# Kernel optimization log

Measured on AMD Instinct MI355X. Metric: run time of the kernel, lower is better.

Reference implementation:

```python
import jax, jax.numpy as jnp
import numpy as np

N, D = 768, 64
EPS = 1e-5

def _ln(x, g, b):
    u = x.mean(-1, keepdims=True)
    s = ((x - u) ** 2).mean(-1, keepdims=True)
    return g * (x - u) / jnp.sqrt(s + EPS) + b

def setup_inputs() -> dict:
    key = jax.random.key(0)
    ks = jax.random.split(key, 16)
    inp = {
        'corr_index': jax.random.normal(ks[0], (N, N, 2), dtype=jnp.float32),
        'nei_index': jax.random.randint(ks[1], (N, N), 0, 2, dtype=jnp.int32),
        'nei_num': jax.random.randint(ks[2], (N,), 0, N, dtype=jnp.int32),
        'hidden_state': jax.random.normal(ks[3], (N, D), dtype=jnp.float32),
        'cn': jax.random.normal(ks[4], (N, D), dtype=jnp.float32),
        # relativeLayer: MLP(2 -> D)
        'W_r': jax.random.normal(ks[5], (2, D)) * 0.01, 'b_r': jnp.zeros((D,)),
        'g_r': jnp.ones((D,)), 'be_r': jax.random.normal(ks[6], (D,)) * 0.02,
        # ngate: MLP_gate(3D -> D)
        'W_g': jax.random.normal(ks[7], (3 * D, D)) * 0.01, 'b_g': jnp.zeros((D,)),
        'g_g': jnp.ones((D,)), 'be_g': jax.random.normal(ks[8], (D,)) * 0.02,
        # WAr: MLP(3D -> 1)
        'W_a': jax.random.normal(ks[9], (3 * D, 1)) * 0.01, 'b_a': jnp.zeros((1,)),
        'g_a': jnp.ones((1,)), 'be_a': jnp.abs(jax.random.normal(ks[10], (1,))) * 0.02 + 0.01,
        # weight: MLP(D -> D)
        'W_w': jax.random.normal(ks[11], (D, D)) * 0.01, 'b_w': jnp.zeros((D,)),
        'g_w': jnp.ones((D,)), 'be_w': jax.random.normal(ks[12], (D,)) * 0.02,
    }
    return inp

def reference(corr_index, nei_index, nei_num, hidden_state, cn,
              W_r, b_r, g_r, be_r, W_g, b_g, g_g, be_g,
              W_a, b_a, g_a, be_a, W_w, b_w, g_w, be_w):
    n, d = hidden_state.shape
    mask = nei_index > 0  # [N,N]; (i,j): j is neighbor of i
    # relativeLayer on all pairs (values at masked positions match the torch gather)
    r = jax.nn.relu(_ln(corr_index @ W_r + b_r, g_r, be_r))  # [N,N,D]
    hi = jnp.broadcast_to(hidden_state[:, None, :], (n, n, d))  # hi_t: h[i]
    hj = jnp.broadcast_to(hidden_state[None, :, :], (n, n, d))  # nei_inputs: h[j]
    tmp = jnp.concatenate([r, hi, hj], axis=-1)  # [N,N,3D]
    nGate = jax.nn.sigmoid(_ln(tmp @ W_g + b_g, g_g, be_g))  # [N,N,D]
    tt = jax.nn.relu(_ln(tmp @ W_a + b_a, g_a, be_a))[..., 0]  # [N,N]
    Pos = jnp.where(mask, tt, 0.0)
    Pos = jnp.where(Pos == 0.0, -10000.0, Pos)  # Pos[Pos==0] = -10000
    Pos = jax.nn.softmax(Pos, axis=1)  # masked row-softmax over neighbors j
    # H[i,j] = h[j] * nGate[i,j] * Pos[i,j] at masked pairs, else 0
    H = jnp.where(mask[..., None], hj * nGate * Pos[..., None], 0.0)
    H_sum = jax.nn.relu(_ln(jnp.sum(H, axis=1) @ W_w + b_w, g_w, be_w))  # [N,D]
    C = H_sum + cn
    H_out = hidden_state + jnp.tanh(C)
    return (H_out, C)
```

## Files before the change

### kernel.cpp

```cpp
#include <hip/hip_runtime.h>


#define NN 768
#define DD 64
#define NCH 12
#define EPSF 1e-5f

typedef __attribute__((ext_vector_type(8))) short short8;
typedef __attribute__((ext_vector_type(4))) float float4v;

__device__ __forceinline__ unsigned short f2bf(float f) {
  unsigned int u = __float_as_uint(f);
  u += 0x7fffu + ((u >> 16) & 1u);
  return (unsigned short)(u >> 16);
}

__global__ __launch_bounds__(256) void prep_kernel(
    const float* __restrict__ hidden, const float* __restrict__ Wg,
    const float* __restrict__ bg, const float* __restrict__ Wr,
    const float* __restrict__ br, const int* __restrict__ nei,
    float* __restrict__ A_pre, float* __restrict__ B_pre,
    float* __restrict__ w0h, float* __restrict__ w1h, float* __restrict__ bh,
    float* __restrict__ evec, unsigned short* __restrict__ WgT,
    unsigned short* __restrict__ Lst, int* __restrict__ cnt_g) {
  const int bid = blockIdx.x;
  const int tid = threadIdx.x;

  if (bid < NN) {
    __shared__ int cLds;
    if (tid == 0) cLds = 0;
    __syncthreads();
#pragma unroll
    for (int rep = 0; rep < 3; ++rep) {
      int jj = tid + rep * 256;
      if (nei[bid * NN + jj] > 0) {
        int idx = atomicAdd(&cLds, 1);
        Lst[bid * NN + idx] = (unsigned short)jj;
      }
    }
    __syncthreads();
    if (tid == 0) cnt_g[bid] = cLds;
    return;
  }

  if (bid == NN) {
    for (int idx = tid; idx < DD * DD; idx += 256) {
      int n = idx >> 6, k = idx & 63;
      WgT[idx] = f2bf(Wg[k * DD + n]);
    }
    if (tid < 64) {
      int t = tid;
      float w0 = Wr[t], w1 = Wr[DD + t], bb = br[t];
      float m0 = w0, m1 = w1, mb = bb;
      for (int m = 1; m < 64; m <<= 1) {
        m0 += __shfl_xor(m0, m);
        m1 += __shfl_xor(m1, m);
        mb += __shfl_xor(mb, m);
      }
      m0 *= (1.f / DD);
      m1 *= (1.f / DD);
      mb *= (1.f / DD);
      float a0 = w0 - m0, a1 = w1 - m1, ab = bb - mb;
      w0h[t] = a0;
      w1h[t] = a1;
      bh[t] = ab;
      float e00 = a0 * a0, e11 = a1 * a1, ebb = ab * ab;
      float e01 = a0 * a1, e0b = a0 * ab, e1b = a1 * ab;
      for (int m = 1; m < 64; m <<= 1) {
        e00 += __shfl_xor(e00, m);
        e11 += __shfl_xor(e11, m);
        ebb += __shfl_xor(ebb, m);
        e01 += __shfl_xor(e01, m);
        e0b += __shfl_xor(e0b, m);
        e1b += __shfl_xor(e1b, m);
      }
      if (t == 0) {
        evec[0] = e00 * (1.f / DD);
        evec[1] = e11 * (1.f / DD);
        evec[2] = ebb * (1.f / DD);
        evec[3] = e01 * (1.f / DD);
        evec[4] = e0b * (1.f / DD);
        evec[5] = e1b * (1.f / DD);
      }
    }
    return;
  }

  const int w = tid >> 6;
  const int lane = tid & 63;
  const int i = (bid - NN - 1) * 4 + w;
  float hv = hidden[i * DD + lane];
  float a = bg[lane];
  float b = 0.f;
#pragma unroll 8
  for (int k = 0; k < DD; ++k) {
    float hk = __shfl(hv, k);
    a = fmaf(hk, Wg[(DD + k) * DD + lane], a);
    b = fmaf(hk, Wg[(2 * DD + k) * DD + lane], b);
  }
  A_pre[i * DD + lane] = a;
  B_pre[i * DD + lane] = b;
}

__global__ __launch_bounds__(64) void pair_kernel(
    const float* __restrict__ corr, const float* __restrict__ hidden,
    const float* __restrict__ gr, const float* __restrict__ ber,
    const float* __restrict__ gg, const float* __restrict__ beg,
    const float* __restrict__ A_pre, const float* __restrict__ B_pre,
    const float* __restrict__ w0h, const float* __restrict__ w1h,
    const float* __restrict__ bh, const float* __restrict__ evec,
    const unsigned short* __restrict__ WgT,
    const unsigned short* __restrict__ Lst, const int* __restrict__ cnt_g,
    float* __restrict__ Hpart) {
  const int bid = blockIdx.x;
  const int i = bid / NCH;
  const int c = bid - i * NCH;
  const int cnt = cnt_g[i];
  const int base = c * 64;
  if (base >= cnt) return;

  const int lane = threadIdx.x;
  const int quad = lane >> 4;
  const int nl = lane & 15;

  __shared__ __align__(16) unsigned short Rt[64 * 72];
  __shared__ int jpc[64];

  int pg = base + lane;
  int jp = (int)Lst[i * NN + (pg < cnt ? pg : base)];
  jpc[lane] = jp;
  float c0 = corr[(i * NN + jp) * 2 + 0];
  float c1 = corr[(i * NN + jp) * 2 + 1];
  const float e00 = evec[0], e11 = evec[1], ebb = evec[2];
  const float e01 = evec[3], e0b = evec[4], e1b = evec[5];
  float var = c0 * c0 * e00 + c1 * c1 * e11 + ebb +
              2.f * (c0 * c1 * e01 + c0 * e0b + c1 * e1b);
  float iv = rsqrtf(var + EPSF);

  const float pgr = gr[lane];
  const float gw0 = pgr * w0h[lane];
  const float gw1 = pgr * w1h[lane];
  const float gbh = pgr * bh[lane];
  const float pber = ber[lane];

  short8 Bf[2][4];
#pragma unroll
  for (int ks = 0; ks < 2; ++ks)
#pragma unroll
    for (int nt = 0; nt < 4; ++nt)
      __builtin_memcpy(&Bf[ks][nt], &WgT[(nt * 16 + nl) * DD + ks * 32 + quad * 8],
                       16);

  float gg4[4], beg4[4], pre4[4];
#pragma unroll
  for (int nt = 0; nt < 4; ++nt) {
    int d = nt * 16 + nl;
    gg4[nt] = gg[d];
    beg4[nt] = beg[d];
    pre4[nt] = A_pre[i * DD + d];
  }

#pragma unroll
  for (int p = 0; p < 64; ++p) {
    float sc0 = __shfl(c0, p);
    float sc1 = __shfl(c1, p);
    float siv = __shfl(iv, p);
    float s3 = fmaf(sc0, gw0, fmaf(sc1, gw1, gbh));
    float r = fmaxf(0.f, fmaf(siv, s3, pber));
    Rt[p * 72 + lane] = f2bf(r);
  }
  __syncthreads();

  float accT[4] = {0.f, 0.f, 0.f, 0.f};

#pragma unroll
  for (int t = 0; t < 4; ++t) {
    short8 a0, a1;
    __builtin_memcpy(&a0, &Rt[(t * 16 + nl) * 72 + quad * 8], 16);
    __builtin_memcpy(&a1, &Rt[(t * 16 + nl) * 72 + 32 + quad * 8], 16);
    float4v acc[4];
#pragma unroll
    for (int nt = 0; nt < 4; ++nt) {
      float4v z = {0.f, 0.f, 0.f, 0.f};
      z = __builtin_amdgcn_mfma_f32_16x16x32_bf16(a0, Bf[0][nt], z, 0, 0, 0);
      z = __builtin_amdgcn_mfma_f32_16x16x32_bf16(a1, Bf[1][nt], z, 0, 0, 0);
      acc[nt] = z;
    }

    int jpr[4];
    float pv[4];
#pragma unroll
    for (int rr = 0; rr < 4; ++rr) {
      int pl = t * 16 + quad * 4 + rr;
      jpr[rr] = jpc[pl];
      pv[rr] = (base + pl < cnt) ? 1.f : 0.f;
    }
    float y[4][4];
#pragma unroll
    for (int nt = 0; nt < 4; ++nt)
#pragma unroll
      for (int rr = 0; rr < 4; ++rr)
        y[nt][rr] = acc[nt][rr] + pre4[nt] + B_pre[jpr[rr] * DD + nt * 16 + nl];
#pragma unroll
    for (int rr = 0; rr < 4; ++rr) {
      float s = y[0][rr] + y[1][rr] + y[2][rr] + y[3][rr];
      float qq = y[0][rr] * y[0][rr] + y[1][rr] * y[1][rr] +
                 y[2][rr] * y[2][rr] + y[3][rr] * y[3][rr];
#pragma unroll
      for (int m = 1; m < 16; m <<= 1) {
        s += __shfl_xor(s, m);
        qq += __shfl_xor(qq, m);
      }
      float u = s * (1.f / DD);
      float vv = qq * (1.f / DD) - u * u;
      float inv = rsqrtf(vv + EPSF);
      int jj = jpr[rr];
#pragma unroll
      for (int nt = 0; nt < 4; ++nt) {
        float g = fmaf(gg4[nt], (y[nt][rr] - u) * inv, beg4[nt]);
        float gate = __frcp_rn(1.f + __expf(-g));
        float hval = hidden[jj * DD + nt * 16 + nl];
        accT[nt] = fmaf(gate * pv[rr], hval, accT[nt]);
      }
    }
  }

#pragma unroll
  for (int nt = 0; nt < 4; ++nt) {
    accT[nt] += __shfl_xor(accT[nt], 16);
    accT[nt] += __shfl_xor(accT[nt], 32);
  }
  if (lane < 16) {
#pragma unroll
    for (int nt = 0; nt < 4; ++nt)
      Hpart[bid * DD + nt * 16 + nl] = accT[nt];
  }
}

__global__ __launch_bounds__(64) void final_kernel(
    const float* __restrict__ hidden, const float* __restrict__ cn,
    const float* __restrict__ bea, const float* __restrict__ Ww,
    const float* __restrict__ bw, const float* __restrict__ gw,
    const float* __restrict__ bew, const int* __restrict__ cnt_g,
    const float* __restrict__ Hpart, float* __restrict__ out) {
  const int i = blockIdx.x;
  const int d = threadIdx.x;
  const int cnt = cnt_g[i];
  const int nch = (cnt + 63) >> 6;
  float hs = 0.f;
  for (int c = 0; c < nch; ++c) hs += Hpart[(i * NCH + c) * DD + d];
  float tta = fmaxf(bea[0], 0.f);
  float wgt = (tta > 0.f && cnt > 0) ? (1.f / (float)cnt) : (1.f / (float)NN);
  hs *= wgt;

  float dotv = bw[d];
#pragma unroll 8
  for (int k = 0; k < DD; ++k) {
    float hk = __shfl(hs, k);
    dotv = fmaf(hk, Ww[k * DD + d], dotv);
  }
  float s = dotv, qq = dotv * dotv;
#pragma unroll
  for (int m = 1; m < 64; m <<= 1) {
    s += __shfl_xor(s, m);
    qq += __shfl_xor(qq, m);
  }
  float u = s * (1.f / DD);
  float var = qq * (1.f / DD) - u * u;
  float inv = rsqrtf(var + EPSF);
  float val = fmaxf(0.f, fmaf(gw[d], (dotv - u) * inv, bew[d]));
  float Cv = val + cn[i * DD + d];
  float Ho = hidden[i * DD + d] + tanhf(Cv);
  out[i * DD + d] = Ho;
  out[NN * DD + i * DD + d] = Cv;
}

extern "C" void kernel_launch(void* const* d_in, const int* in_sizes, int n_in,
                              void* d_out, int out_size, void* d_ws,
                              size_t ws_size, hipStream_t stream) {
  const float* corr = (const float*)d_in[0];
  const int* nei = (const int*)d_in[1];
  const float* hidden = (const float*)d_in[3];
  const float* cn = (const float*)d_in[4];
  const float* Wr = (const float*)d_in[5];
  const float* br = (const float*)d_in[6];
  const float* gr = (const float*)d_in[7];
  const float* ber = (const float*)d_in[8];
  const float* Wg = (const float*)d_in[9];
  const float* bg = (const float*)d_in[10];
  const float* gg = (const float*)d_in[11];
  const float* beg = (const float*)d_in[12];
  const float* bea = (const float*)d_in[16];
  const float* Ww = (const float*)d_in[17];
  const float* bw = (const float*)d_in[18];
  const float* gw = (const float*)d_in[19];
  const float* bew = (const float*)d_in[20];
  float* out = (float*)d_out;

  float* ws = (float*)d_ws;
  float* A_pre = ws;
  float* B_pre = ws + 49152;
  float* w0h = ws + 98304;
  float* w1h = ws + 98368;
  float* bh = ws + 98432;
  float* evec = ws + 98496;
  unsigned short* WgT = (unsigned short*)(ws + 98512);
  int* cnt_g = (int*)(ws + 100560);
  unsigned short* Lst = (unsigned short*)(ws + 101328);
  float* Hpart = ws + 396240;

  prep_kernel<<<NN + 1 + NN / 4, 256, 0, stream>>>(
      hidden, Wg, bg, Wr, br, nei, A_pre, B_pre, w0h, w1h, bh, evec, WgT, Lst,
      cnt_g);
  pair_kernel<<<NN * NCH, 64, 0, stream>>>(corr, hidden, gr, ber, gg, beg,
                                           A_pre, B_pre, w0h, w1h, bh, evec,
                                           WgT, Lst, cnt_g, Hpart);
  final_kernel<<<NN, 64, 0, stream>>>(hidden, cn, bea, Ww, bw, gw, bew, cnt_g,
                                      Hpart, out);
}
```

Measured before the change: 141.2 us.

## Restructure pair kernel into 32-pair wave chunks with interleaved B/hidden loads

The pair kernel now gives each wave a 32-neighbor chunk, with four waves per 256-thread block. This replaces one 64-pair chunk per 64-thread block. Each lane computes half a row of the relative-layer activations directly into LDS, instead of broadcasting per-pair values with shuffles. B_pre and hidden are interleaved into one float2 array so a single gather fetches both. The LN/gate constants are also packed into vector arrays. The intent is better occupancy and load balance for rows with few neighbors, and fewer shuffles and separate gathers. In exchange there are more partial sums for the final kernel to reduce, and the code relies on a wave-local fence in place of a barrier.

```diff
diff --git a/kernel.cpp b/kernel.cpp
--- a/kernel.cpp
+++ b/kernel.cpp
@@ -3,11 +3,13 @@
 
 #define NN 768
 #define DD 64
-#define NCH 12
+#define CHP 32
+#define NCH 24
 #define EPSF 1e-5f
 
 typedef __attribute__((ext_vector_type(8))) short short8;
 typedef __attribute__((ext_vector_type(4))) float float4v;
+typedef __attribute__((ext_vector_type(2))) float float2v;
 
 __device__ __forceinline__ unsigned short f2bf(float f) {
   unsigned int u = __float_as_uint(f);
@@ -18,9 +20,11 @@
 __global__ __launch_bounds__(256) void prep_kernel(
     const float* __restrict__ hidden, const float* __restrict__ Wg,
     const float* __restrict__ bg, const float* __restrict__ Wr,
-    const float* __restrict__ br, const int* __restrict__ nei,
-    float* __restrict__ A_pre, float* __restrict__ B_pre,
-    float* __restrict__ w0h, float* __restrict__ w1h, float* __restrict__ bh,
+    const float* __restrict__ br, const float* __restrict__ gr,
+    const float* __restrict__ ber, const float* __restrict__ gg,
+    const float* __restrict__ beg, const int* __restrict__ nei,
+    float* __restrict__ A_pre, float2v* __restrict__ BH,
+    float4v* __restrict__ KT, float2v* __restrict__ GB,
     float* __restrict__ evec, unsigned short* __restrict__ WgT,
     unsigned short* __restrict__ Lst, int* __restrict__ cnt_g) {
   const int bid = blockIdx.x;
@@ -61,9 +65,17 @@
       m1 *= (1.f / DD);
       mb *= (1.f / DD);
       float a0 = w0 - m0, a1 = w1 - m1, ab = bb - mb;
-      w0h[t] = a0;
-      w1h[t] = a1;
-      bh[t] = ab;
+      float grt = gr[t];
+      float4v kt;
+      kt[0] = grt * a0;
+      kt[1] = grt * a1;
+      kt[2] = grt * ab;
+      kt[3] = ber[t];
+      KT[t] = kt;
+      float2v gb;
+      gb[0] = gg[t];
+      gb[1] = beg[t];
+      GB[t] = gb;
       float e00 = a0 * a0, e11 = a1 * a1, ebb = ab * ab;
       float e01 = a0 * a1, e0b = a0 * ab, e1b = a1 * ab;
       for (int m = 1; m < 64; m <<= 1) {
@@ -99,85 +111,84 @@
     b = fmaf(hk, Wg[(2 * DD + k) * DD + lane], b);
   }
   A_pre[i * DD + lane] = a;
-  B_pre[i * DD + lane] = b;
-}
-
-__global__ __launch_bounds__(64) void pair_kernel(
-    const float* __restrict__ corr, const float* __restrict__ hidden,
-    const float* __restrict__ gr, const float* __restrict__ ber,
-    const float* __restrict__ gg, const float* __restrict__ beg,
-    const float* __restrict__ A_pre, const float* __restrict__ B_pre,
-    const float* __restrict__ w0h, const float* __restrict__ w1h,
-    const float* __restrict__ bh, const float* __restrict__ evec,
+  float2v bh2;
+  bh2[0] = b;
+  bh2[1] = hv;
+  BH[i * DD + lane] = bh2;
+}
+
+__global__ __launch_bounds__(256) void pair_kernel(
+    const float2v* __restrict__ corr2, const float* __restrict__ A_pre,
+    const float2v* __restrict__ BH, const float4v* __restrict__ KT,
+    const float2v* __restrict__ GB, const float* __restrict__ evec,
     const unsigned short* __restrict__ WgT,
     const unsigned short* __restrict__ Lst, const int* __restrict__ cnt_g,
     float* __restrict__ Hpart) {
-  const int bid = blockIdx.x;
-  const int i = bid / NCH;
-  const int c = bid - i * NCH;
+  __shared__ __align__(16) unsigned short Rt[4][CHP * 72];
+
+  const int b = blockIdx.x;
+  const int tid = threadIdx.x;
+  const int wid = tid >> 6;
+  const int i = b / 6;
+  const int c = (b - i * 6) * 4 + wid;
   const int cnt = cnt_g[i];
-  const int base = c * 64;
+  const int base = c * CHP;
   if (base >= cnt) return;
 
-  const int lane = threadIdx.x;
+  const int lane = tid & 63;
   const int quad = lane >> 4;
   const int nl = lane & 15;
-
-  __shared__ __align__(16) unsigned short Rt[64 * 72];
-  __shared__ int jpc[64];
-
-  int pg = base + lane;
+  const int p32 = lane & 31;
+  const int h = lane >> 5;
+
+  int pg = base + p32;
   int jp = (int)Lst[i * NN + (pg < cnt ? pg : base)];
-  jpc[lane] = jp;
-  float c0 = corr[(i * NN + jp) * 2 + 0];
-  float c1 = corr[(i * NN + jp) * 2 + 1];
+  float2v cc = corr2[i * NN + jp];
   const float e00 = evec[0], e11 = evec[1], ebb = evec[2];
   const float e01 = evec[3], e0b = evec[4], e1b = evec[5];
-  float var = c0 * c0 * e00 + c1 * c1 * e11 + ebb +
-              2.f * (c0 * c1 * e01 + c0 * e0b + c1 * e1b);
+  float var = cc[0] * cc[0] * e00 + cc[1] * cc[1] * e11 + ebb +
+              2.f * (cc[0] * cc[1] * e01 + cc[0] * e0b + cc[1] * e1b);
   float iv = rsqrtf(var + EPSF);
 
-  const float pgr = gr[lane];
-  const float gw0 = pgr * w0h[lane];
-  const float gw1 = pgr * w1h[lane];
-  const float gbh = pgr * bh[lane];
-  const float pber = ber[lane];
-
   short8 Bf[2][4];
 #pragma unroll
   for (int ks = 0; ks < 2; ++ks)
 #pragma unroll
     for (int nt = 0; nt < 4; ++nt)
-      __builtin_memcpy(&Bf[ks][nt], &WgT[(nt * 16 + nl) * DD + ks * 32 + quad * 8],
-                       16);
+      __builtin_memcpy(&Bf[ks][nt],
+                       &WgT[(nt * 16 + nl) * DD + ks * 32 + quad * 8], 16);
 
   float gg4[4], beg4[4], pre4[4];
 #pragma unroll
   for (int nt = 0; nt < 4; ++nt) {
     int d = nt * 16 + nl;
-    gg4[nt] = gg[d];
-    beg4[nt] = beg[d];
+    float2v gb = GB[d];
+    gg4[nt] = gb[0];
+    beg4[nt] = gb[1];
     pre4[nt] = A_pre[i * DD + d];
   }
 
-#pragma unroll
-  for (int p = 0; p < 64; ++p) {
-    float sc0 = __shfl(c0, p);
-    float sc1 = __shfl(c1, p);
-    float siv = __shfl(iv, p);
-    float s3 = fmaf(sc0, gw0, fmaf(sc1, gw1, gbh));
-    float r = fmaxf(0.f, fmaf(siv, s3, pber));
-    Rt[p * 72 + lane] = f2bf(r);
-  }
-  __syncthreads();
+  {
+    short8 wbuf;
+#pragma unroll
+    for (int kk = 0; kk < 32; ++kk) {
+      float4v kt = KT[h * 32 + kk];
+      float s3 = fmaf(cc[0], kt[0], fmaf(cc[1], kt[1], kt[2]));
+      float r = fmaxf(0.f, fmaf(iv, s3, kt[3]));
+      wbuf[kk & 7] = (short)f2bf(r);
+      if ((kk & 7) == 7)
+        __builtin_memcpy(&Rt[wid][p32 * 72 + h * 32 + (kk & ~7)], &wbuf, 16);
+    }
+  }
+  __builtin_amdgcn_fence(__ATOMIC_ACQ_REL, "workgroup");
 
   float accT[4] = {0.f, 0.f, 0.f, 0.f};
 
 #pragma unroll
-  for (int t = 0; t < 4; ++t) {
+  for (int t = 0; t < 2; ++t) {
     short8 a0, a1;
-    __builtin_memcpy(&a0, &Rt[(t * 16 + nl) * 72 + quad * 8], 16);
-    __builtin_memcpy(&a1, &Rt[(t * 16 + nl) * 72 + 32 + quad * 8], 16);
+    __builtin_memcpy(&a0, &Rt[wid][(t * 16 + nl) * 72 + quad * 8], 16);
+    __builtin_memcpy(&a1, &Rt[wid][(t * 16 + nl) * 72 + 32 + quad * 8], 16);
     float4v acc[4];
 #pragma unroll
     for (int nt = 0; nt < 4; ++nt) {
@@ -192,15 +203,22 @@
 #pragma unroll
     for (int rr = 0; rr < 4; ++rr) {
       int pl = t * 16 + quad * 4 + rr;
-      jpr[rr] = jpc[pl];
+      jpr[rr] = __shfl(jp, pl);
       pv[rr] = (base + pl < cnt) ? 1.f : 0.f;
     }
+    float2v bh2[4][4];
+#pragma unroll
+    for (int rr = 0; rr < 4; ++rr)
+#pragma unroll
+      for (int nt = 0; nt < 4; ++nt)
+        bh2[rr][nt] = BH[jpr[rr] * DD + nt * 16 + nl];
+
     float y[4][4];
 #pragma unroll
     for (int nt = 0; nt < 4; ++nt)
 #pragma unroll
       for (int rr = 0; rr < 4; ++rr)
-        y[nt][rr] = acc[nt][rr] + pre4[nt] + B_pre[jpr[rr] * DD + nt * 16 + nl];
+        y[nt][rr] = acc[nt][rr] + pre4[nt] + bh2[rr][nt][0];
 #pragma unroll
     for (int rr = 0; rr < 4; ++rr) {
       float s = y[0][rr] + y[1][rr] + y[2][rr] + y[3][rr];
@@ -214,13 +232,11 @@
       float u = s * (1.f / DD);
       float vv = qq * (1.f / DD) - u * u;
       float inv = rsqrtf(vv + EPSF);
-      int jj = jpr[rr];
 #pragma unroll
       for (int nt = 0; nt < 4; ++nt) {
         float g = fmaf(gg4[nt], (y[nt][rr] - u) * inv, beg4[nt]);
         float gate = __frcp_rn(1.f + __expf(-g));
-        float hval = hidden[jj * DD + nt * 16 + nl];
-        accT[nt] = fmaf(gate * pv[rr], hval, accT[nt]);
+        accT[nt] = fmaf(gate * pv[rr], bh2[rr][nt][1], accT[nt]);
       }
     }
   }
@@ -233,7 +249,7 @@
   if (lane < 16) {
 #pragma unroll
     for (int nt = 0; nt < 4; ++nt)
-      Hpart[bid * DD + nt * 16 + nl] = accT[nt];
+      Hpart[(i * NCH + c) * DD + nt * 16 + nl] = accT[nt];
   }
 }
 
@@ -246,7 +262,7 @@
   const int i = blockIdx.x;
   const int d = threadIdx.x;
   const int cnt = cnt_g[i];
-  const int nch = (cnt + 63) >> 6;
+  const int nch = (cnt + CHP - 1) >> 5;
   float hs = 0.f;
   for (int c = 0; c < nch; ++c) hs += Hpart[(i * NCH + c) * DD + d];
   float tta = fmaxf(bea[0], 0.f);
@@ -299,22 +315,20 @@
 
   float* ws = (float*)d_ws;
   float* A_pre = ws;
-  float* B_pre = ws + 49152;
-  float* w0h = ws + 98304;
-  float* w1h = ws + 98368;
-  float* bh = ws + 98432;
-  float* evec = ws + 98496;
-  unsigned short* WgT = (unsigned short*)(ws + 98512);
-  int* cnt_g = (int*)(ws + 100560);
-  unsigned short* Lst = (unsigned short*)(ws + 101328);
-  float* Hpart = ws + 396240;
+  float2v* BH = (float2v*)(ws + 49152);
+  float4v* KT = (float4v*)(ws + 147456);
+  float2v* GB = (float2v*)(ws + 147712);
+  float* evec = ws + 147840;
+  unsigned short* WgT = (unsigned short*)(ws + 147856);
+  int* cnt_g = (int*)(ws + 149904);
+  unsigned short* Lst = (unsigned short*)(ws + 150672);
+  float* Hpart = ws + 445584;
 
   prep_kernel<<<NN + 1 + NN / 4, 256, 0, stream>>>(
-      hidden, Wg, bg, Wr, br, nei, A_pre, B_pre, w0h, w1h, bh, evec, WgT, Lst,
-      cnt_g);
-  pair_kernel<<<NN * NCH, 64, 0, stream>>>(corr, hidden, gr, ber, gg, beg,
-                                           A_pre, B_pre, w0h, w1h, bh, evec,
-                                           WgT, Lst, cnt_g, Hpart);
+      hidden, Wg, bg, Wr, br, gr, ber, gg, beg, nei, A_pre, BH, KT, GB, evec,
+      WgT, Lst, cnt_g);
+  pair_kernel<<<NN * 6, 256, 0, stream>>>((const float2v*)corr, A_pre, BH, KT,
+                                          GB, evec, WgT, Lst, cnt_g, Hpart);
   final_kernel<<<NN, 64, 0, stream>>>(hidden, cn, bea, Ww, bw, gw, bew, cnt_g,
                                       Hpart, out);
 }
```

After: 150.3 us. 6.4% more time.
